# Kernel tuning notes

Measured on AMD Instinct MI355X. Metric: run time of the kernel, lower is better.

## Reference

```python
import jax, jax.numpy as jnp
import numpy as np

NUM_HEADS = 16


def setup_inputs() -> dict:
    key = jax.random.key(0)
    k1, k2, k3 = jax.random.split(key, 3)
    B, S, C = 1, 4096, 1024
    x = jax.random.normal(k1, (B, S, C), dtype=jnp.float32)
    # additive causal mask: 0 on/below diagonal, -1e9 above
    causal = jnp.triu(jnp.full((S, S), -1e9, dtype=jnp.float32), k=1)
    attention_mask = causal[None, None, :, :]
    W_attn = jax.random.normal(k2, (C, 3 * C), dtype=jnp.float32) * (C ** -0.5)
    b_attn = jnp.zeros((3 * C,), dtype=jnp.float32)
    W_proj = jax.random.normal(k3, (C, C), dtype=jnp.float32) * (C ** -0.5)
    b_proj = jnp.zeros((C,), dtype=jnp.float32)
    return {"x": x, "attention_mask": attention_mask, "W_attn": W_attn,
            "b_attn": b_attn, "W_proj": W_proj, "b_proj": b_proj}


def reference(x, attention_mask, W_attn, b_attn, W_proj, b_proj):
    B, S, C = x.shape
    H = NUM_HEADS
    hd = C // H
    qkv = x @ W_attn + b_attn                      # [B,S,3C]
    q, k, v = jnp.split(qkv, 3, axis=-1)
    # [B,S,C] -> [B,H,S,hd]
    q = q.reshape(B, S, H, hd).transpose(0, 2, 1, 3)
    k = k.reshape(B, S, H, hd).transpose(0, 2, 1, 3)
    v = v.reshape(B, S, H, hd).transpose(0, 2, 1, 3)
    att = jnp.einsum('bhqd,bhkd->bhqk', q, k) / jnp.sqrt(jnp.float32(hd))
    att = att + attention_mask                     # additive causal mask
    att = jax.nn.softmax(att, axis=-1)             # dropout is identity (p=0/eval)
    out = jnp.einsum('bhqk,bhkd->bhqd', att, v)    # [B,H,S,hd]
    out = out.transpose(0, 2, 1, 3).reshape(B, S, C)
    return out @ W_proj + b_proj
```

## Files before the change

### kernel.cpp

```cpp
#include <hip/hip_runtime.h>
#include <stdint.h>


typedef __bf16 bf16x8 __attribute__((ext_vector_type(8)));
typedef float f32x4 __attribute__((ext_vector_type(4)));

#define QSCALE 0.18033688011112042f

__device__ __forceinline__ f32x4 mfma16(bf16x8 a, bf16x8 b, f32x4 c) {
  return __builtin_amdgcn_mfma_f32_16x16x32_bf16(a, b, c, 0, 0, 0);
}

__device__ __forceinline__ void g2l16(const void* g, void* l) {
  __builtin_amdgcn_global_load_lds(
      (const __attribute__((address_space(1))) unsigned int*)g,
      (__attribute__((address_space(3))) unsigned int*)l,
      16, 0, 0);
}

__device__ __forceinline__ uint16_t f2bf(float f) {
  unsigned int u = __builtin_bit_cast(unsigned int, f);
  u += 0x7fffu + ((u >> 16) & 1u);
  return (uint16_t)(u >> 16);
}

__device__ __forceinline__ unsigned int pack_hi(float lo, float hi) {
  return __builtin_amdgcn_perm(__builtin_bit_cast(unsigned int, hi),
                               __builtin_bit_cast(unsigned int, lo), 0x07060302u);
}

__global__ __launch_bounds__(256) void f2b_k(const float* __restrict__ in,
                                             uint16_t* __restrict__ out, int n) {
  const int base = (blockIdx.x * 256 + threadIdx.x) * 8;
  if (base >= n) return;
  float4 a = *(const float4*)(in + base);
  float4 b = *(const float4*)(in + base + 4);
  uint16_t t[8];
  t[0] = f2bf(a.x); t[1] = f2bf(a.y); t[2] = f2bf(a.z); t[3] = f2bf(a.w);
  t[4] = f2bf(b.x); t[5] = f2bf(b.y); t[6] = f2bf(b.z); t[7] = f2bf(b.w);
  *(int4*)(out + base) = *(const int4*)t;
}

__global__ __launch_bounds__(256) void transpose2_f2b(const float* __restrict__ inA,
                                                      uint16_t* __restrict__ outA,
                                                      const float* __restrict__ inB,
                                                      uint16_t* __restrict__ outB) {
  __shared__ float t[64][65];
  const int tx = threadIdx.x & 15;
  const int ty = threadIdx.x >> 4;
  const bool isA = blockIdx.x < 48;
  const float* in = isA ? inA : inB;
  uint16_t* out = isA ? outA : outB;
  const int C = isA ? 3072 : 1024;
  const int bx = isA ? blockIdx.x : (blockIdx.x - 48);
  const int r0 = blockIdx.y * 64, c0 = bx * 64;
#pragma unroll
  for (int rr = ty; rr < 64; rr += 16) {
    float4 v = *(const float4*)(in + (size_t)(r0 + rr) * C + c0 + tx * 4);
    t[rr][tx * 4 + 0] = v.x; t[rr][tx * 4 + 1] = v.y;
    t[rr][tx * 4 + 2] = v.z; t[rr][tx * 4 + 3] = v.w;
  }
  __syncthreads();
#pragma unroll
  for (int cc = ty; cc < 64; cc += 16) {
    uint16_t tmp[4];
#pragma unroll
    for (int j = 0; j < 4; j++) tmp[j] = f2bf(t[tx * 4 + j][cc]);
    *(uint2*)(out + (size_t)(c0 + cc) * 1024 + r0 + tx * 4) = *(const uint2*)tmp;
  }
}

template <int EPI>
__global__ __launch_bounds__(256) void gemm_bt(const uint16_t* __restrict__ A,
                                               const uint16_t* __restrict__ Bt,
                                               const float* __restrict__ bias,
                                               uint16_t* __restrict__ outQ,
                                               uint16_t* __restrict__ outK,
                                               uint16_t* __restrict__ outV,
                                               float* __restrict__ outF) {
  __shared__ __align__(16) uint16_t lA[128 * 32];
  __shared__ __align__(16) uint16_t lB[128 * 32];
  const int tid = threadIdx.x;
  const int w = tid >> 6, lane = tid & 63;
  const int quad = lane >> 4, c16 = lane & 15;
  const int m0 = blockIdx.y * 128, n0 = blockIdx.x * 128;

  f32x4 acc[4][4];
#pragma unroll
  for (int i = 0; i < 4; i++)
#pragma unroll
    for (int j = 0; j < 4; j++) acc[i][j] = f32x4{0.f, 0.f, 0.f, 0.f};

  for (int k0 = 0; k0 < 1024; k0 += 32) {
    __syncthreads();
#pragma unroll
    for (int ii = 0; ii < 2; ii++) {
      const int instr = w * 2 + ii;
      const int p16 = instr * 64 + lane;
      const int row = p16 >> 2, cp = p16 & 3;
      const int c = cp ^ ((row >> 1) & 3);
      g2l16(A + (size_t)(m0 + row) * 1024 + k0 + c * 8, (char*)lA + (size_t)instr * 1024);
      g2l16(Bt + (size_t)(n0 + row) * 1024 + k0 + c * 8, (char*)lB + (size_t)instr * 1024);
    }
    __syncthreads();
    bf16x8 af[4], bfr[4];
#pragma unroll
    for (int t = 0; t < 4; t++) {
      const int mr = (w >> 1) * 64 + t * 16 + c16;
      af[t] = *(const bf16x8*)((const char*)lA + mr * 64 + ((quad ^ ((mr >> 1) & 3)) * 16));
      const int nr = (w & 1) * 64 + t * 16 + c16;
      bfr[t] = *(const bf16x8*)((const char*)lB + nr * 64 + ((quad ^ ((nr >> 1) & 3)) * 16));
    }
#pragma unroll
    for (int i = 0; i < 4; i++)
#pragma unroll
      for (int j = 0; j < 4; j++) acc[i][j] = mfma16(af[i], bfr[j], acc[i][j]);
  }

  const int mbase = m0 + (w >> 1) * 64;
  const int nbase = n0 + (w & 1) * 64;
  float bv[4];
#pragma unroll
  for (int j = 0; j < 4; j++) bv[j] = bias[nbase + j * 16 + c16];
#pragma unroll
  for (int i = 0; i < 4; i++) {
#pragma unroll
    for (int j = 0; j < 4; j++) {
      const int n = nbase + j * 16 + c16;
#pragma unroll
      for (int r = 0; r < 4; r++) {
        const int m = mbase + i * 16 + quad * 4 + r;
        float fv = acc[i][j][r] + bv[j];
        if (EPI == 0) {
          const int region = n >> 10;
          const int cr = n & 1023;
          const int h = cr >> 6, d = cr & 63;
          if (region == 0)      outQ[((size_t)(h << 12) + m) * 64 + d] = f2bf(fv * QSCALE);
          else if (region == 1) outK[((size_t)(h << 12) + m) * 64 + d] = f2bf(fv);
          else                  outV[(((size_t)(h * 32 + (m >> 7)) * 64 + d) << 7) + (m & 127)] = f2bf(fv);
        } else {
          outF[(size_t)m * 1024 + n] = fv;
        }
      }
    }
  }
}

__global__ __launch_bounds__(256, 2) void attn_kernel(const uint16_t* __restrict__ Qb,
                                                      const uint16_t* __restrict__ Kb,
                                                      const uint16_t* __restrict__ Vtb,
                                                      uint16_t* __restrict__ Ob) {
  __shared__ __align__(16) uint16_t lP[4][64 * 128];
  __shared__ float lL[4][64];
  const int tid = threadIdx.x;
  const int w = tid >> 6;
  const int lane = tid & 63;
  const int quad = lane >> 4, c16 = lane & 15;
  const int bid = blockIdx.x;
  const int h = bid & 15;
  const int sw = 63 - (bid >> 4);
  const int q0w = sw * 64;
  const int jmax = sw >> 1;

  bf16x8 qf[4][2];
#pragma unroll
  for (int ntq = 0; ntq < 4; ntq++)
#pragma unroll
    for (int kc = 0; kc < 2; kc++) {
      int4 v = *(const int4*)(Qb + ((size_t)(h << 12) + q0w + ntq * 16 + c16) * 64 + kc * 32 + quad * 8);
      qf[ntq][kc] = __builtin_bit_cast(bf16x8, v);
    }

  float ls[4] = {0.f, 0.f, 0.f, 0.f};
  f32x4 o[4][4];
#pragma unroll
  for (int i = 0; i < 4; i++)
#pragma unroll
    for (int nq = 0; nq < 4; nq++) o[i][nq] = f32x4{0.f, 0.f, 0.f, 0.f};

  for (int j = w; j <= jmax; j += 4) {
    const uint16_t* kbase = Kb + ((size_t)(h << 12) + j * 128) * 64;

#pragma unroll
    for (int half = 0; half < 2; half++) {
      int4 kf[2][4];
#pragma unroll
      for (int kc = 0; kc < 2; kc++)
#pragma unroll
        for (int mt = 0; mt < 4; mt++)
          kf[kc][mt] = *(const int4*)(kbase + (half * 64 + mt * 16 + c16) * 64 + kc * 32 + quad * 8);

#pragma unroll
      for (int qp = 0; qp < 2; qp++) {
        f32x4 st[4][2];
#pragma unroll
        for (int mt = 0; mt < 4; mt++) { st[mt][0] = f32x4{0.f,0.f,0.f,0.f}; st[mt][1] = f32x4{0.f,0.f,0.f,0.f}; }
#pragma unroll
        for (int kc = 0; kc < 2; kc++)
#pragma unroll
          for (int mt = 0; mt < 4; mt++) {
            bf16x8 a = __builtin_bit_cast(bf16x8, kf[kc][mt]);
            st[mt][0] = mfma16(a, qf[qp * 2 + 0][kc], st[mt][0]);
            st[mt][1] = mfma16(a, qf[qp * 2 + 1][kc], st[mt][1]);
          }

        if (j == jmax) {
#pragma unroll
          for (int nt = 0; nt < 2; nt++) {
            const int qg = q0w + qp * 32 + nt * 16 + c16;
#pragma unroll
            for (int mt = 0; mt < 4; mt++)
#pragma unroll
              for (int rr = 0; rr < 4; rr++) {
                const int key = j * 128 + half * 64 + mt * 16 + quad * 4 + rr;
                if (key > qg) st[mt][nt][rr] = -1.0e9f;
              }
          }
        }

#pragma unroll
        for (int nt = 0; nt < 2; nt++) {
          float sum0 = 0.f, sum1 = 0.f;
          const int prow = qp * 32 + nt * 16 + c16;
          const size_t pbase = (size_t)prow * 256;
#pragma unroll
          for (int mt = 0; mt < 4; mt++) {
            float p0 = __builtin_amdgcn_exp2f(st[mt][nt][0]);
            float p1 = __builtin_amdgcn_exp2f(st[mt][nt][1]);
            float p2 = __builtin_amdgcn_exp2f(st[mt][nt][2]);
            float p3 = __builtin_amdgcn_exp2f(st[mt][nt][3]);
            sum0 += p0 + p1;
            sum1 += p2 + p3;
            const unsigned int lo = pack_hi(p0, p1);
            const unsigned int hi = pack_hi(p2, p3);
            const int chunk = half * 8 + mt * 2 + (quad >> 1);
            uint2* dst = (uint2*)((char*)lP[w] + pbase + ((chunk ^ (prow & 15)) << 4) + (quad & 1) * 8);
            *dst = make_uint2(lo, hi);
          }
          float sum = sum0 + sum1;
          sum += __shfl_xor(sum, 16);
          sum += __shfl_xor(sum, 32);
          ls[qp * 2 + nt] += sum;
        }
      }
    }

    const uint16_t* vbase = Vtb + (((size_t)(h * 32 + j) * 64) << 7);
#pragma unroll
    for (int kc = 0; kc < 4; kc++) {
      int4 vf[4];
#pragma unroll
      for (int mt = 0; mt < 4; mt++)
        vf[mt] = *(const int4*)(vbase + ((mt * 16 + c16) << 7) + (kc * 4 + quad) * 8);
      bf16x8 pb[4];
#pragma unroll
      for (int ntq = 0; ntq < 4; ntq++) {
        const int prow = ntq * 16 + c16;
        const int chunk = kc * 4 + quad;
        pb[ntq] = *(const bf16x8*)((const char*)lP[w] + (size_t)prow * 256 +
                                   ((chunk ^ (prow & 15)) << 4));
      }
#pragma unroll
      for (int mt = 0; mt < 4; mt++) {
        bf16x8 a = __builtin_bit_cast(bf16x8, vf[mt]);
#pragma unroll
        for (int ntq = 0; ntq < 4; ntq++)
          o[mt][ntq] = mfma16(a, pb[ntq], o[mt][ntq]);
      }
    }
  }

  float* oL = (float*)lP[w];
#pragma unroll
  for (int mt = 0; mt < 4; mt++)
#pragma unroll
    for (int ntq = 0; ntq < 4; ntq++)
#pragma unroll
      for (int rr = 0; rr < 4; rr++)
        oL[(mt * 16 + quad * 4 + rr) * 64 + ntq * 16 + c16] = o[mt][ntq][rr];
  if (quad == 0) {
#pragma unroll
    for (int ntq = 0; ntq < 4; ntq++) lL[w][ntq * 16 + c16] = ls[ntq];
  }
  __syncthreads();

  const int q = tid & 63, dq = tid >> 6;
  const float lsum = lL[0][q] + lL[1][q] + lL[2][q] + lL[3][q];
  const float inv = 1.f / lsum;
  uint16_t t[16] __attribute__((aligned(16)));
#pragma unroll
  for (int i = 0; i < 16; i++) {
    const int d = dq * 16 + i;
    const int off = d * 64 + q;
    float s = ((const float*)lP[0])[off] + ((const float*)lP[1])[off] +
              ((const float*)lP[2])[off] + ((const float*)lP[3])[off];
    t[i] = f2bf(s * inv);
  }
  uint16_t* dst = Ob + (size_t)(q0w + q) * 1024 + h * 64 + dq * 16;
  *(int4*)dst = *(const int4*)t;
  *(int4*)(dst + 8) = *(const int4*)(t + 8);
}

extern "C" void kernel_launch(void* const* d_in, const int* in_sizes, int n_in,
                              void* d_out, int out_size, void* d_ws, size_t ws_size,
                              hipStream_t stream) {
  const float* x      = (const float*)d_in[0];
  const float* W_attn = (const float*)d_in[2];
  const float* b_attn = (const float*)d_in[3];
  const float* W_proj = (const float*)d_in[4];
  const float* b_proj = (const float*)d_in[5];
  float* out = (float*)d_out;

  char* ws = (char*)d_ws;
  uint16_t* Ob  = (uint16_t*)(ws);
  uint16_t* wtA = (uint16_t*)(ws + 8388608);
  uint16_t* wtP = (uint16_t*)(ws + 14680064);
  uint16_t* Qb  = (uint16_t*)(ws + 16777216);
  uint16_t* Kb  = (uint16_t*)(ws + 25165824);
  uint16_t* Vtb = (uint16_t*)(ws + 33554432);
  uint16_t* xb  = (uint16_t*)(ws + 41943040);

  f2b_k<<<2048, 256, 0, stream>>>(x, xb, 4096 * 1024);
  transpose2_f2b<<<dim3(64, 16), 256, 0, stream>>>(W_attn, wtA, W_proj, wtP);
  gemm_bt<0><<<dim3(24, 32), 256, 0, stream>>>(xb, wtA, b_attn, Qb, Kb, Vtb, nullptr);
  attn_kernel<<<dim3(1024), 256, 0, stream>>>(Qb, Kb, Vtb, Ob);
  gemm_bt<1><<<dim3(8, 32), 256, 0, stream>>>(Ob, wtP, b_proj, nullptr, nullptr, nullptr, out);
}
```

Baseline: 262.0 us.

## Pair causal query tiles per block with 8 waves over 64-key tiles

The attention kernel now launches 512 blocks of 512 threads. Each block handles two query tiles, a long one and its mirrored short one, so the causal work per block is balanced. Keys are split across 8 waves in 64-key steps instead of 4 waves in 128-key steps, which shrinks the per-wave P buffer. Partial outputs are combined through a tree reduction in shared memory with swizzled vector stores. The costs are more __syncthreads calls, a second phase per block, and higher register pressure from the 512-thread launch bound.

```diff
diff --git a/kernel.cpp b/kernel.cpp
--- a/kernel.cpp
+++ b/kernel.cpp
@@ -146,49 +146,50 @@
   }
 }
 
-__global__ __launch_bounds__(256, 2) void attn_kernel(const uint16_t* __restrict__ Qb,
+__global__ __launch_bounds__(512, 4) void attn_kernel(const uint16_t* __restrict__ Qb,
                                                       const uint16_t* __restrict__ Kb,
                                                       const uint16_t* __restrict__ Vtb,
                                                       uint16_t* __restrict__ Ob) {
-  __shared__ __align__(16) uint16_t lP[4][64 * 128];
-  __shared__ float lL[4][64];
+  __shared__ __align__(16) uint16_t lP[8][64 * 64];
+  __shared__ float lL[8][64];
   const int tid = threadIdx.x;
-  const int w = tid >> 6;
+  const int v = tid >> 6;
   const int lane = tid & 63;
   const int quad = lane >> 4, c16 = lane & 15;
   const int bid = blockIdx.x;
   const int h = bid & 15;
-  const int sw = 63 - (bid >> 4);
-  const int q0w = sw * 64;
-  const int jmax = sw >> 1;
-
-  bf16x8 qf[4][2];
-#pragma unroll
-  for (int ntq = 0; ntq < 4; ntq++)
-#pragma unroll
-    for (int kc = 0; kc < 2; kc++) {
-      int4 v = *(const int4*)(Qb + ((size_t)(h << 12) + q0w + ntq * 16 + c16) * 64 + kc * 32 + quad * 8);
-      qf[ntq][kc] = __builtin_bit_cast(bf16x8, v);
-    }
-
-  float ls[4] = {0.f, 0.f, 0.f, 0.f};
-  f32x4 o[4][4];
-#pragma unroll
-  for (int i = 0; i < 4; i++)
-#pragma unroll
-    for (int nq = 0; nq < 4; nq++) o[i][nq] = f32x4{0.f, 0.f, 0.f, 0.f};
-
-  for (int j = w; j <= jmax; j += 4) {
-    const uint16_t* kbase = Kb + ((size_t)(h << 12) + j * 128) * 64;
-
-#pragma unroll
-    for (int half = 0; half < 2; half++) {
+  const int p = bid >> 4;
+
+  for (int phase = 0; phase < 2; ++phase) {
+    const int s = phase ? p : (63 - p);
+    const int vsel = phase ? (7 - v) : v;
+    const int q0w = s * 64;
+
+    bf16x8 qf[4][2];
+#pragma unroll
+    for (int ntq = 0; ntq < 4; ntq++)
+#pragma unroll
+      for (int kc = 0; kc < 2; kc++) {
+        int4 vv = *(const int4*)(Qb + ((size_t)(h << 12) + q0w + ntq * 16 + c16) * 64 + kc * 32 + quad * 8);
+        qf[ntq][kc] = __builtin_bit_cast(bf16x8, vv);
+      }
+
+    float ls[4] = {0.f, 0.f, 0.f, 0.f};
+    f32x4 o[4][4];
+#pragma unroll
+    for (int i = 0; i < 4; i++)
+#pragma unroll
+      for (int nq = 0; nq < 4; nq++) o[i][nq] = f32x4{0.f, 0.f, 0.f, 0.f};
+
+    for (int hh = vsel; hh <= s; hh += 8) {
+      const uint16_t* kbase = Kb + ((size_t)(h << 12) + hh * 64) * 64;
+
       int4 kf[2][4];
 #pragma unroll
       for (int kc = 0; kc < 2; kc++)
 #pragma unroll
         for (int mt = 0; mt < 4; mt++)
-          kf[kc][mt] = *(const int4*)(kbase + (half * 64 + mt * 16 + c16) * 64 + kc * 32 + quad * 8);
+          kf[kc][mt] = *(const int4*)(kbase + (mt * 16 + c16) * 64 + kc * 32 + quad * 8);
 
 #pragma unroll
       for (int qp = 0; qp < 2; qp++) {
@@ -204,16 +205,16 @@
             st[mt][1] = mfma16(a, qf[qp * 2 + 1][kc], st[mt][1]);
           }
 
-        if (j == jmax) {
+        if (hh == s) {
 #pragma unroll
           for (int nt = 0; nt < 2; nt++) {
-            const int qg = q0w + qp * 32 + nt * 16 + c16;
+            const int qloc = qp * 32 + nt * 16 + c16;
 #pragma unroll
             for (int mt = 0; mt < 4; mt++)
 #pragma unroll
               for (int rr = 0; rr < 4; rr++) {
-                const int key = j * 128 + half * 64 + mt * 16 + quad * 4 + rr;
-                if (key > qg) st[mt][nt][rr] = -1.0e9f;
+                const int key = mt * 16 + quad * 4 + rr;
+                if (key > qloc) st[mt][nt][rr] = -1.0e9f;
               }
           }
         }
@@ -222,7 +223,7 @@
         for (int nt = 0; nt < 2; nt++) {
           float sum0 = 0.f, sum1 = 0.f;
           const int prow = qp * 32 + nt * 16 + c16;
-          const size_t pbase = (size_t)prow * 256;
+          const size_t pbase = (size_t)prow * 128;
 #pragma unroll
           for (int mt = 0; mt < 4; mt++) {
             float p0 = __builtin_amdgcn_exp2f(st[mt][nt][0]);
@@ -233,8 +234,8 @@
             sum1 += p2 + p3;
             const unsigned int lo = pack_hi(p0, p1);
             const unsigned int hi = pack_hi(p2, p3);
-            const int chunk = half * 8 + mt * 2 + (quad >> 1);
-            uint2* dst = (uint2*)((char*)lP[w] + pbase + ((chunk ^ (prow & 15)) << 4) + (quad & 1) * 8);
+            const int chunk = mt * 2 + (quad >> 1);
+            uint2* dst = (uint2*)((char*)lP[v] + pbase + ((chunk ^ (prow & 7)) << 4) + (quad & 1) * 8);
             *dst = make_uint2(lo, hi);
           }
           float sum = sum0 + sum1;
@@ -243,62 +244,95 @@
           ls[qp * 2 + nt] += sum;
         }
       }
-    }
-
-    const uint16_t* vbase = Vtb + (((size_t)(h * 32 + j) * 64) << 7);
-#pragma unroll
-    for (int kc = 0; kc < 4; kc++) {
-      int4 vf[4];
-#pragma unroll
-      for (int mt = 0; mt < 4; mt++)
-        vf[mt] = *(const int4*)(vbase + ((mt * 16 + c16) << 7) + (kc * 4 + quad) * 8);
-      bf16x8 pb[4];
-#pragma unroll
-      for (int ntq = 0; ntq < 4; ntq++) {
-        const int prow = ntq * 16 + c16;
-        const int chunk = kc * 4 + quad;
-        pb[ntq] = *(const bf16x8*)((const char*)lP[w] + (size_t)prow * 256 +
-                                   ((chunk ^ (prow & 15)) << 4));
+
+      const int jt = hh >> 1;
+      const uint16_t* vbase = Vtb + (((size_t)(h * 32 + jt) * 64) << 7);
+#pragma unroll
+      for (int kc = 0; kc < 2; kc++) {
+        int4 vf[4];
+#pragma unroll
+        for (int mt = 0; mt < 4; mt++)
+          vf[mt] = *(const int4*)(vbase + ((mt * 16 + c16) << 7) + ((hh & 1) * 8 + kc * 4 + quad) * 8);
+        bf16x8 pb[4];
+#pragma unroll
+        for (int ntq = 0; ntq < 4; ntq++) {
+          const int prow = ntq * 16 + c16;
+          const int chunk = kc * 4 + quad;
+          pb[ntq] = *(const bf16x8*)((const char*)lP[v] + (size_t)prow * 128 +
+                                     ((chunk ^ (prow & 7)) << 4));
+        }
+#pragma unroll
+        for (int mt = 0; mt < 4; mt++) {
+          bf16x8 a = __builtin_bit_cast(bf16x8, vf[mt]);
+#pragma unroll
+          for (int ntq = 0; ntq < 4; ntq++)
+            o[mt][ntq] = mfma16(a, pb[ntq], o[mt][ntq]);
+        }
       }
-#pragma unroll
-      for (int mt = 0; mt < 4; mt++) {
-        bf16x8 a = __builtin_bit_cast(bf16x8, vf[mt]);
-#pragma unroll
-        for (int ntq = 0; ntq < 4; ntq++)
-          o[mt][ntq] = mfma16(a, pb[ntq], o[mt][ntq]);
-      }
-    }
-  }
-
-  float* oL = (float*)lP[w];
-#pragma unroll
-  for (int mt = 0; mt < 4; mt++)
-#pragma unroll
-    for (int ntq = 0; ntq < 4; ntq++)
-#pragma unroll
-      for (int rr = 0; rr < 4; rr++)
-        oL[(mt * 16 + quad * 4 + rr) * 64 + ntq * 16 + c16] = o[mt][ntq][rr];
-  if (quad == 0) {
-#pragma unroll
-    for (int ntq = 0; ntq < 4; ntq++) lL[w][ntq * 16 + c16] = ls[ntq];
-  }
-  __syncthreads();
-
-  const int q = tid & 63, dq = tid >> 6;
-  const float lsum = lL[0][q] + lL[1][q] + lL[2][q] + lL[3][q];
-  const float inv = 1.f / lsum;
-  uint16_t t[16] __attribute__((aligned(16)));
-#pragma unroll
-  for (int i = 0; i < 16; i++) {
-    const int d = dq * 16 + i;
-    const int off = d * 64 + q;
-    float s = ((const float*)lP[0])[off] + ((const float*)lP[1])[off] +
-              ((const float*)lP[2])[off] + ((const float*)lP[3])[off];
-    t[i] = f2bf(s * inv);
-  }
-  uint16_t* dst = Ob + (size_t)(q0w + q) * 1024 + h * 64 + dq * 16;
-  *(int4*)dst = *(const int4*)t;
-  *(int4*)(dst + 8) = *(const int4*)(t + 8);
+    }
+
+    if (quad == 0) {
+#pragma unroll
+      for (int ntq = 0; ntq < 4; ntq++) lL[v][ntq * 16 + c16] = ls[ntq];
+    }
+
+    char* base = (char*)lP;
+#define SPILL_O(region)                                                         \
+  {                                                                             \
+    float* oL = (float*)(base + (region) * 16384);                              \
+    _Pragma("unroll") for (int mt = 0; mt < 4; mt++)                            \
+        _Pragma("unroll") for (int ntq = 0; ntq < 4; ntq++) {                   \
+      const int q = ntq * 16 + c16;                                             \
+      const int db = mt * 16 + quad * 4;                                        \
+      *(f32x4*)(oL + q * 64 + (db ^ ((q & 7) << 3))) = o[mt][ntq];              \
+    }                                                                           \
+  }
+#define ADD_O(region)                                                           \
+  {                                                                             \
+    const float* oL = (const float*)(base + (region) * 16384);                  \
+    _Pragma("unroll") for (int mt = 0; mt < 4; mt++)                            \
+        _Pragma("unroll") for (int ntq = 0; ntq < 4; ntq++) {                   \
+      const int q = ntq * 16 + c16;                                             \
+      const int db = mt * 16 + quad * 4;                                        \
+      o[mt][ntq] += *(const f32x4*)(oL + q * 64 + (db ^ ((q & 7) << 3)));       \
+    }                                                                           \
+  }
+    __syncthreads();
+    if (v >= 4) SPILL_O(v - 4);
+    __syncthreads();
+    if (v < 4) ADD_O(v);
+    __syncthreads();
+    if (v == 2 || v == 3) SPILL_O(v - 2);
+    __syncthreads();
+    if (v < 2) ADD_O(v);
+    __syncthreads();
+    if (v < 2) SPILL_O(v);
+    __syncthreads();
+
+    {
+      const int q = tid & 63, dg = tid >> 6;
+      float lsum = 0.f;
+#pragma unroll
+      for (int i = 0; i < 8; i++) lsum += lL[i][q];
+      const float inv = 1.f / lsum;
+      const float* r0 = (const float*)base;
+      const float* r1 = (const float*)(base + 16384);
+      const int off = q * 64 + ((dg ^ (q & 7)) << 3);
+      f32x4 a0 = *(const f32x4*)(r0 + off);
+      f32x4 a1 = *(const f32x4*)(r0 + off + 4);
+      f32x4 b0 = *(const f32x4*)(r1 + off);
+      f32x4 b1 = *(const f32x4*)(r1 + off + 4);
+      uint16_t t[8] __attribute__((aligned(16)));
+#pragma unroll
+      for (int i = 0; i < 4; i++) t[i] = f2bf((a0[i] + b0[i]) * inv);
+#pragma unroll
+      for (int i = 0; i < 4; i++) t[4 + i] = f2bf((a1[i] + b1[i]) * inv);
+      *(int4*)(Ob + (size_t)(q0w + q) * 1024 + h * 64 + dg * 8) = *(const int4*)t;
+    }
+    if (phase == 0) __syncthreads();
+  }
+#undef SPILL_O
+#undef ADD_O
 }
 
 extern "C" void kernel_launch(void* const* d_in, const int* in_sizes, int n_in,
@@ -323,6 +357,6 @@
   f2b_k<<<2048, 256, 0, stream>>>(x, xb, 4096 * 1024);
   transpose2_f2b<<<dim3(64, 16), 256, 0, stream>>>(W_attn, wtA, W_proj, wtP);
   gemm_bt<0><<<dim3(24, 32), 256, 0, stream>>>(xb, wtA, b_attn, Qb, Kb, Vtb, nullptr);
-  attn_kernel<<<dim3(1024), 256, 0, stream>>>(Qb, Kb, Vtb, Ob);
+  attn_kernel<<<dim3(512), 512, 0, stream>>>(Qb, Kb, Vtb, Ob);
   gemm_bt<1><<<dim3(8, 32), 256, 0, stream>>>(Ob, wtP, b_proj, nullptr, nullptr, nullptr, out);
 }
```

Result: slower. 385.2 us (+47.1%).

## Software-pipeline K/V register loads across halves and iterations in attention loop

Applied to the files above, without the earlier changes.

Restructures the attention inner loop so the next K half-tile, and the next iteration's first K half-tile, are loaded into registers while the current QK/softmax and PV MFMAs run. PV is split per half, so V loads for each half are issued ahead of their use. The goal is to hide global-load latency behind compute. The cost is higher VGPR pressure from double-buffered K/V fragments, which could lower occupancy or cause spills.

```diff
diff --git a/kernel.cpp b/kernel.cpp
--- a/kernel.cpp
+++ b/kernel.cpp
@@ -178,97 +178,114 @@
 #pragma unroll
     for (int nq = 0; nq < 4; nq++) o[i][nq] = f32x4{0.f, 0.f, 0.f, 0.f};
 
+#define LOAD_K(KF, KBASE, HALF)                                                 \
+  _Pragma("unroll") for (int kc = 0; kc < 2; kc++)                              \
+      _Pragma("unroll") for (int mt = 0; mt < 4; mt++)                          \
+          KF[kc][mt] = *(const int4*)((KBASE) + ((HALF) * 64 + mt * 16 + c16) * 64 + kc * 32 + quad * 8);
+
+#define LOAD_V(VF, HALF)                                                        \
+  _Pragma("unroll") for (int kc2 = 0; kc2 < 2; kc2++)                           \
+      _Pragma("unroll") for (int mt = 0; mt < 4; mt++)                          \
+          VF[kc2][mt] = *(const int4*)(vbase + ((mt * 16 + c16) << 7) +         \
+                                       ((HALF) * 8 + kc2 * 4 + quad) * 8);
+
+#define QK_SOFTMAX(HALF, KF)                                                    \
+  _Pragma("unroll") for (int qp = 0; qp < 2; qp++) {                            \
+    f32x4 st[4][2];                                                             \
+    _Pragma("unroll") for (int mt = 0; mt < 4; mt++) {                          \
+      st[mt][0] = f32x4{0.f, 0.f, 0.f, 0.f};                                    \
+      st[mt][1] = f32x4{0.f, 0.f, 0.f, 0.f};                                    \
+    }                                                                           \
+    _Pragma("unroll") for (int kc = 0; kc < 2; kc++)                            \
+        _Pragma("unroll") for (int mt = 0; mt < 4; mt++) {                      \
+      bf16x8 a = __builtin_bit_cast(bf16x8, KF[kc][mt]);                        \
+      st[mt][0] = mfma16(a, qf[qp * 2 + 0][kc], st[mt][0]);                     \
+      st[mt][1] = mfma16(a, qf[qp * 2 + 1][kc], st[mt][1]);                     \
+    }                                                                           \
+    if (j == jmax) {                                                            \
+      _Pragma("unroll") for (int nt = 0; nt < 2; nt++) {                        \
+        const int qg = q0w + qp * 32 + nt * 16 + c16;                           \
+        _Pragma("unroll") for (int mt = 0; mt < 4; mt++)                        \
+            _Pragma("unroll") for (int rr = 0; rr < 4; rr++) {                  \
+          const int key = j * 128 + (HALF) * 64 + mt * 16 + quad * 4 + rr;      \
+          if (key > qg) st[mt][nt][rr] = -1.0e9f;                               \
+        }                                                                       \
+      }                                                                         \
+    }                                                                           \
+    _Pragma("unroll") for (int nt = 0; nt < 2; nt++) {                          \
+      float sum0 = 0.f, sum1 = 0.f;                                             \
+      const int prow = qp * 32 + nt * 16 + c16;                                 \
+      const size_t pbase = (size_t)prow * 256;                                  \
+      _Pragma("unroll") for (int mt = 0; mt < 4; mt++) {                        \
+        float p0 = __builtin_amdgcn_exp2f(st[mt][nt][0]);                       \
+        float p1 = __builtin_amdgcn_exp2f(st[mt][nt][1]);                       \
+        float p2 = __builtin_amdgcn_exp2f(st[mt][nt][2]);                       \
+        float p3 = __builtin_amdgcn_exp2f(st[mt][nt][3]);                       \
+        sum0 += p0 + p1;                                                        \
+        sum1 += p2 + p3;                                                        \
+        const unsigned int lo = pack_hi(p0, p1);                                \
+        const unsigned int hi = pack_hi(p2, p3);                                \
+        const int chunk = (HALF) * 8 + mt * 2 + (quad >> 1);                    \
+        uint2* dst = (uint2*)((char*)lP[w] + pbase +                            \
+                              ((chunk ^ (prow & 15)) << 4) + (quad & 1) * 8);   \
+        *dst = make_uint2(lo, hi);                                              \
+      }                                                                         \
+      float sum = sum0 + sum1;                                                  \
+      sum += __shfl_xor(sum, 16);                                               \
+      sum += __shfl_xor(sum, 32);                                               \
+      ls[qp * 2 + nt] += sum;                                                   \
+    }                                                                           \
+  }
+
+#define PV_HALF(HALF, VF)                                                       \
+  _Pragma("unroll") for (int kc2 = 0; kc2 < 2; kc2++) {                         \
+    bf16x8 pb[4];                                                               \
+    _Pragma("unroll") for (int ntq = 0; ntq < 4; ntq++) {                       \
+      const int prow = ntq * 16 + c16;                                          \
+      const int chunk = (HALF) * 8 + kc2 * 4 + quad;                            \
+      pb[ntq] = *(const bf16x8*)((const char*)lP[w] + (size_t)prow * 256 +      \
+                                 ((chunk ^ (prow & 15)) << 4));                 \
+    }                                                                           \
+    _Pragma("unroll") for (int mt = 0; mt < 4; mt++) {                          \
+      bf16x8 a = __builtin_bit_cast(bf16x8, VF[kc2][mt]);                       \
+      _Pragma("unroll") for (int ntq = 0; ntq < 4; ntq++)                       \
+          o[mt][ntq] = mfma16(a, pb[ntq], o[mt][ntq]);                          \
+    }                                                                           \
+  }
+
+  int4 kfA[2][4], kfB[2][4], vfA[2][4], vfB[2][4];
+  {
+    const uint16_t* kb0 = Kb + ((size_t)(h << 12) + w * 128) * 64;
+    LOAD_K(kfA, kb0, 0);
+  }
+
   for (int j = w; j <= jmax; j += 4) {
     const uint16_t* kbase = Kb + ((size_t)(h << 12) + j * 128) * 64;
-
-#pragma unroll
-    for (int half = 0; half < 2; half++) {
-      int4 kf[2][4];
-#pragma unroll
-      for (int kc = 0; kc < 2; kc++)
-#pragma unroll
-        for (int mt = 0; mt < 4; mt++)
-          kf[kc][mt] = *(const int4*)(kbase + (half * 64 + mt * 16 + c16) * 64 + kc * 32 + quad * 8);
-
-#pragma unroll
-      for (int qp = 0; qp < 2; qp++) {
-        f32x4 st[4][2];
-#pragma unroll
-        for (int mt = 0; mt < 4; mt++) { st[mt][0] = f32x4{0.f,0.f,0.f,0.f}; st[mt][1] = f32x4{0.f,0.f,0.f,0.f}; }
-#pragma unroll
-        for (int kc = 0; kc < 2; kc++)
-#pragma unroll
-          for (int mt = 0; mt < 4; mt++) {
-            bf16x8 a = __builtin_bit_cast(bf16x8, kf[kc][mt]);
-            st[mt][0] = mfma16(a, qf[qp * 2 + 0][kc], st[mt][0]);
-            st[mt][1] = mfma16(a, qf[qp * 2 + 1][kc], st[mt][1]);
-          }
-
-        if (j == jmax) {
-#pragma unroll
-          for (int nt = 0; nt < 2; nt++) {
-            const int qg = q0w + qp * 32 + nt * 16 + c16;
-#pragma unroll
-            for (int mt = 0; mt < 4; mt++)
-#pragma unroll
-              for (int rr = 0; rr < 4; rr++) {
-                const int key = j * 128 + half * 64 + mt * 16 + quad * 4 + rr;
-                if (key > qg) st[mt][nt][rr] = -1.0e9f;
-              }
-          }
-        }
-
-#pragma unroll
-        for (int nt = 0; nt < 2; nt++) {
-          float sum0 = 0.f, sum1 = 0.f;
-          const int prow = qp * 32 + nt * 16 + c16;
-          const size_t pbase = (size_t)prow * 256;
-#pragma unroll
-          for (int mt = 0; mt < 4; mt++) {
-            float p0 = __builtin_amdgcn_exp2f(st[mt][nt][0]);
-            float p1 = __builtin_amdgcn_exp2f(st[mt][nt][1]);
-            float p2 = __builtin_amdgcn_exp2f(st[mt][nt][2]);
-            float p3 = __builtin_amdgcn_exp2f(st[mt][nt][3]);
-            sum0 += p0 + p1;
-            sum1 += p2 + p3;
-            const unsigned int lo = pack_hi(p0, p1);
-            const unsigned int hi = pack_hi(p2, p3);
-            const int chunk = half * 8 + mt * 2 + (quad >> 1);
-            uint2* dst = (uint2*)((char*)lP[w] + pbase + ((chunk ^ (prow & 15)) << 4) + (quad & 1) * 8);
-            *dst = make_uint2(lo, hi);
-          }
-          float sum = sum0 + sum1;
-          sum += __shfl_xor(sum, 16);
-          sum += __shfl_xor(sum, 32);
-          ls[qp * 2 + nt] += sum;
-        }
-      }
-    }
-
     const uint16_t* vbase = Vtb + (((size_t)(h * 32 + j) * 64) << 7);
-#pragma unroll
-    for (int kc = 0; kc < 4; kc++) {
-      int4 vf[4];
-#pragma unroll
-      for (int mt = 0; mt < 4; mt++)
-        vf[mt] = *(const int4*)(vbase + ((mt * 16 + c16) << 7) + (kc * 4 + quad) * 8);
-      bf16x8 pb[4];
-#pragma unroll
-      for (int ntq = 0; ntq < 4; ntq++) {
-        const int prow = ntq * 16 + c16;
-        const int chunk = kc * 4 + quad;
-        pb[ntq] = *(const bf16x8*)((const char*)lP[w] + (size_t)prow * 256 +
-                                   ((chunk ^ (prow & 15)) << 4));
-      }
-#pragma unroll
-      for (int mt = 0; mt < 4; mt++) {
-        bf16x8 a = __builtin_bit_cast(bf16x8, vf[mt]);
-#pragma unroll
-        for (int ntq = 0; ntq < 4; ntq++)
-          o[mt][ntq] = mfma16(a, pb[ntq], o[mt][ntq]);
-      }
-    }
-  }
+
+    LOAD_V(vfA, 0);
+    LOAD_K(kfB, kbase, 1);
+
+    QK_SOFTMAX(0, kfA);
+
+    {
+      const int jn = (j + 4 <= jmax) ? (j + 4) : j;
+      const uint16_t* kbn = Kb + ((size_t)(h << 12) + jn * 128) * 64;
+      LOAD_K(kfA, kbn, 0);
+    }
+
+    PV_HALF(0, vfA);
+
+    LOAD_V(vfB, 1);
+
+    QK_SOFTMAX(1, kfB);
+    PV_HALF(1, vfB);
+  }
+
+#undef LOAD_K
+#undef LOAD_V
+#undef QK_SOFTMAX
+#undef PV_HALF
 
   float* oL = (float*)lP[w];
 #pragma unroll
```

Measured after the change: 347.2 us. 32.5% more time.

## Interleave PV with QK per half-tile and defer row-sum reduction to epilogue

Applied to the files above, without the earlier changes.

The PV product now runs inside each 64-key half of the tile, right after that half's probabilities are written to LDS, and the V fragments are loaded next to the K fragments so both global loads are in flight together. The per-iteration cross-lane shuffle reduction of softmax row sums is removed. Each quad lane instead keeps a partial sum, and all 16 partials are summed once in the epilogue through a larger LDS array. This shortens dependency chains and cuts shuffle traffic, at the cost of more live registers for V fragments, which may hurt occupancy.

```diff
diff --git a/kernel.cpp b/kernel.cpp
--- a/kernel.cpp
+++ b/kernel.cpp
@@ -151,7 +151,7 @@
                                                       const uint16_t* __restrict__ Vtb,
                                                       uint16_t* __restrict__ Ob) {
   __shared__ __align__(16) uint16_t lP[4][64 * 128];
-  __shared__ float lL[4][64];
+  __shared__ float lL[4][4][64];
   const int tid = threadIdx.x;
   const int w = tid >> 6;
   const int lane = tid & 63;
@@ -180,6 +180,7 @@
 
   for (int j = w; j <= jmax; j += 4) {
     const uint16_t* kbase = Kb + ((size_t)(h << 12) + j * 128) * 64;
+    const uint16_t* vbase = Vtb + (((size_t)(h * 32 + j) * 64) << 7);
 
 #pragma unroll
     for (int half = 0; half < 2; half++) {
@@ -190,11 +191,22 @@
         for (int mt = 0; mt < 4; mt++)
           kf[kc][mt] = *(const int4*)(kbase + (half * 64 + mt * 16 + c16) * 64 + kc * 32 + quad * 8);
 
+      int4 vf[2][4];
+#pragma unroll
+      for (int kc2 = 0; kc2 < 2; kc2++)
+#pragma unroll
+        for (int mt = 0; mt < 4; mt++)
+          vf[kc2][mt] = *(const int4*)(vbase + ((mt * 16 + c16) << 7) +
+                                       (half * 8 + kc2 * 4 + quad) * 8);
+
 #pragma unroll
       for (int qp = 0; qp < 2; qp++) {
         f32x4 st[4][2];
 #pragma unroll
-        for (int mt = 0; mt < 4; mt++) { st[mt][0] = f32x4{0.f,0.f,0.f,0.f}; st[mt][1] = f32x4{0.f,0.f,0.f,0.f}; }
+        for (int mt = 0; mt < 4; mt++) {
+          st[mt][0] = f32x4{0.f, 0.f, 0.f, 0.f};
+          st[mt][1] = f32x4{0.f, 0.f, 0.f, 0.f};
+        }
 #pragma unroll
         for (int kc = 0; kc < 2; kc++)
 #pragma unroll
@@ -237,38 +249,33 @@
             uint2* dst = (uint2*)((char*)lP[w] + pbase + ((chunk ^ (prow & 15)) << 4) + (quad & 1) * 8);
             *dst = make_uint2(lo, hi);
           }
-          float sum = sum0 + sum1;
-          sum += __shfl_xor(sum, 16);
-          sum += __shfl_xor(sum, 32);
-          ls[qp * 2 + nt] += sum;
+          ls[qp * 2 + nt] += sum0 + sum1;
         }
       }
-    }
-
-    const uint16_t* vbase = Vtb + (((size_t)(h * 32 + j) * 64) << 7);
-#pragma unroll
-    for (int kc = 0; kc < 4; kc++) {
-      int4 vf[4];
-#pragma unroll
-      for (int mt = 0; mt < 4; mt++)
-        vf[mt] = *(const int4*)(vbase + ((mt * 16 + c16) << 7) + (kc * 4 + quad) * 8);
-      bf16x8 pb[4];
-#pragma unroll
-      for (int ntq = 0; ntq < 4; ntq++) {
-        const int prow = ntq * 16 + c16;
-        const int chunk = kc * 4 + quad;
-        pb[ntq] = *(const bf16x8*)((const char*)lP[w] + (size_t)prow * 256 +
-                                   ((chunk ^ (prow & 15)) << 4));
+
+#pragma unroll
+      for (int kc2 = 0; kc2 < 2; kc2++) {
+        bf16x8 pb[4];
+#pragma unroll
+        for (int ntq = 0; ntq < 4; ntq++) {
+          const int prow = ntq * 16 + c16;
+          const int chunk = half * 8 + kc2 * 4 + quad;
+          pb[ntq] = *(const bf16x8*)((const char*)lP[w] + (size_t)prow * 256 +
+                                     ((chunk ^ (prow & 15)) << 4));
+        }
+#pragma unroll
+        for (int mt = 0; mt < 4; mt++) {
+          bf16x8 a = __builtin_bit_cast(bf16x8, vf[kc2][mt]);
+#pragma unroll
+          for (int ntq = 0; ntq < 4; ntq++)
+            o[mt][ntq] = mfma16(a, pb[ntq], o[mt][ntq]);
+        }
       }
-#pragma unroll
-      for (int mt = 0; mt < 4; mt++) {
-        bf16x8 a = __builtin_bit_cast(bf16x8, vf[mt]);
-#pragma unroll
-        for (int ntq = 0; ntq < 4; ntq++)
-          o[mt][ntq] = mfma16(a, pb[ntq], o[mt][ntq]);
-      }
-    }
-  }
+    }
+  }
+
+#pragma unroll
+  for (int ntq = 0; ntq < 4; ntq++) lL[w][quad][ntq * 16 + c16] = ls[ntq];
 
   float* oL = (float*)lP[w];
 #pragma unroll
@@ -278,14 +285,14 @@
 #pragma unroll
       for (int rr = 0; rr < 4; rr++)
         oL[(mt * 16 + quad * 4 + rr) * 64 + ntq * 16 + c16] = o[mt][ntq][rr];
-  if (quad == 0) {
-#pragma unroll
-    for (int ntq = 0; ntq < 4; ntq++) lL[w][ntq * 16 + c16] = ls[ntq];
-  }
   __syncthreads();
 
   const int q = tid & 63, dq = tid >> 6;
-  const float lsum = lL[0][q] + lL[1][q] + lL[2][q] + lL[3][q];
+  float lsum = 0.f;
+#pragma unroll
+  for (int i = 0; i < 4; i++)
+#pragma unroll
+    for (int g = 0; g < 4; g++) lsum += lL[i][g][q];
   const float inv = 1.f / lsum;
   uint16_t t[16] __attribute__((aligned(16)));
 #pragma unroll
```

Measured after the change: 358.1 us. +36.7%, slower.
